# Kernel tuning notes

Measured on AMD Instinct MI355X. Metric: run time of the kernel, lower is better.

## Reference

```python
import jax, jax.numpy as jnp
import numpy as np

B, L, IN_DIM, OUT_DIM = 4, 512, 32, 1
D_MODEL, N_LAYERS = 768, 4
E = 2 * D_MODEL      # d_inner
N = 16               # d_state
K = 4                # d_conv
R = D_MODEL // 16    # dt_rank


def setup_inputs() -> dict:
    key = jax.random.key(0)
    ks = jax.random.split(key, 16)
    p = lambda k, shape, s=0.02: (s * jax.random.normal(k, shape)).astype(jnp.float32)
    inp = {
        'x': jax.random.normal(ks[0], (B, L, IN_DIM), dtype=jnp.float32),
        'in_w': p(ks[1], (D_MODEL, IN_DIM)),
        'in_b': jnp.zeros((D_MODEL,), jnp.float32),
        'in_proj_w': p(ks[2], (N_LAYERS, 2 * E, D_MODEL)),
        'conv_w': p(ks[3], (N_LAYERS, E, K), 0.1),
        'conv_b': jnp.zeros((N_LAYERS, E), jnp.float32),
        'xproj_w': p(ks[4], (N_LAYERS, R + 2 * N, E)),
        'dtproj_w': p(ks[5], (N_LAYERS, E, R), 0.1),
        'dtproj_b': p(ks[6], (N_LAYERS, E), 0.5),
        'A_log': jnp.log(jnp.broadcast_to(jnp.arange(1, N + 1, dtype=jnp.float32), (N_LAYERS, E, N))),
        'D_ssm': jnp.ones((N_LAYERS, E), jnp.float32),
        'outproj_w': p(ks[7], (N_LAYERS, D_MODEL, E)),
        'norm_w': jnp.ones((N_LAYERS, D_MODEL), jnp.float32),
        'normf_w': jnp.ones((D_MODEL,), jnp.float32),
        'out_w': p(ks[8], (OUT_DIM, D_MODEL)),
        'out_b': jnp.zeros((OUT_DIM,), jnp.float32),
    }
    return inp


def _rmsnorm(x, w, eps=1e-5):
    return x * jax.lax.rsqrt(jnp.mean(x * x, axis=-1, keepdims=True) + eps) * w


def _selective_scan(u, delta, A, Bm, C, D):
    # u, delta: [B,L,E]; A: [E,N]; Bm, C: [B,L,N]; D: [E]
    dA = jnp.exp(delta[..., None] * A)                       # [B,L,E,N]
    dBu = delta[..., None] * Bm[:, :, None, :] * u[..., None]  # [B,L,E,N]

    def step(h, inp):
        dA_t, dBu_t, C_t = inp
        h = dA_t * h + dBu_t                                  # [B,E,N]
        y = jnp.einsum('ben,bn->be', h, C_t)
        return h, y

    h0 = jnp.zeros((u.shape[0], u.shape[2], A.shape[1]), u.dtype)
    _, ys = jax.lax.scan(step, h0, (dA.transpose(1, 0, 2, 3), dBu.transpose(1, 0, 2, 3), C.transpose(1, 0, 2)))
    return ys.transpose(1, 0, 2) + u * D                      # [B,L,E]


def _mamba_block(xn, in_proj_w, conv_w, conv_b, xproj_w, dtproj_w, dtproj_b, A_log, D_ssm, outproj_w):
    xz = xn @ in_proj_w.T                                     # [B,L,2E]
    xc, res = xz[..., :E], xz[..., E:]
    # depthwise causal conv1d
    xt = xc.transpose(0, 2, 1)                                # [B,E,L]
    y = jax.lax.conv_general_dilated(xt, conv_w[:, None, :], (1,), [(K - 1, 0)],
                                     feature_group_count=E,
                                     dimension_numbers=('NCH', 'OIH', 'NCH'))
    u = jax.nn.silu((y + conv_b[None, :, None]).transpose(0, 2, 1))  # [B,L,E]
    x_dbl = u @ xproj_w.T                                     # [B,L,R+2N]
    dt, Bm, C = x_dbl[..., :R], x_dbl[..., R:R + N], x_dbl[..., R + N:]
    delta = jax.nn.softplus(dt @ dtproj_w.T + dtproj_b)       # [B,L,E]
    A = -jnp.exp(A_log)                                       # [E,N]
    y = _selective_scan(u, delta, A, Bm, C, D_ssm)
    y = y * jax.nn.silu(res)
    return y @ outproj_w.T                                    # [B,L,D_MODEL]


def reference(x, in_w, in_b, in_proj_w, conv_w, conv_b, xproj_w, dtproj_w, dtproj_b,
              A_log, D_ssm, outproj_w, norm_w, normf_w, out_w, out_b):
    h = x @ in_w.T + in_b                                     # [B,L,D_MODEL]
    for i in range(N_LAYERS):
        h = h + _mamba_block(_rmsnorm(h, norm_w[i]), in_proj_w[i], conv_w[i], conv_b[i],
                             xproj_w[i], dtproj_w[i], dtproj_b[i], A_log[i], D_ssm[i], outproj_w[i])
    h = _rmsnorm(h, normf_w)
    last = h[:, -1, :]
    out = jax.nn.sigmoid(last @ out_w.T + out_b)              # [B,OUT_DIM]
    return out.reshape(-1)
```

## Files before the change

kernel.cpp:

```cpp
#include <hip/hip_runtime.h>
#include <hip/hip_bf16.h>
#include <cmath>

#define BATCH 4
#define SEQ 512
#define TOK (BATCH*SEQ)
#define DMODEL 768
#define EDIM 1536
#define TWOE 3072
#define RDIM 48
#define NSTATE 16
#define RN2 80
#define CONVK 4
#define XSPLIT 6
#define CH 8
#define CL (SEQ/CH)
#define EBLK 64

#define EPI_STORE 0
#define EPI_BIAS 1
#define EPI_BIAS_SOFTPLUS 2
#define EPI_ADD 3

typedef short bf16x8 __attribute__((ext_vector_type(8)));
typedef float f32x4 __attribute__((ext_vector_type(4)));

__device__ __forceinline__ unsigned short f2bf(float f) {
  unsigned int u = __builtin_bit_cast(unsigned int, f);
  u = (u + 0x7FFFu + ((u >> 16) & 1u)) >> 16;
  return (unsigned short)u;
}

template<int BM, int BN, int EPI, bool NB>
__global__ __launch_bounds__(256) void gemm_mfma(
    const unsigned short* __restrict__ Abf,
    const unsigned short* __restrict__ Wbf,
    float* __restrict__ C, int ldc, int Kk, int ldk,
    int Nvalid, size_t zCstride, const float* __restrict__ bias) {
  constexpr int WM = BM / 2, WN = BN / 2;
  constexpr int IT = WM / 16, JT = WN / 16;
  __shared__ __align__(16) char smem[(BM + BN) * 128];
  char* ldsA = smem;
  char* ldsB = smem + BM * 128;

  const int tid = threadIdx.x;
  const int wid = tid >> 6, lane = tid & 63;
  const int m0 = blockIdx.y * BM, n0 = blockIdx.x * BN;
  const int wm = (wid >> 1) * WM, wn = (wid & 1) * WN;
  const int quad = lane >> 4, l15 = lane & 15;

  const int srow = lane >> 3;
  const int kc = (lane & 7) ^ srow;
  const int koff = blockIdx.z * Kk;
  C += (size_t)blockIdx.z * zCstride;
  const unsigned short* gA = Abf + (size_t)(m0 + srow) * ldk + kc * 8 + koff;
  const unsigned short* gB = Wbf + (size_t)(n0 + srow) * ldk + kc * 8 + koff;

  f32x4 acc[IT][JT] = {};

  for (int k0 = 0; k0 < Kk; k0 += 64) {
#pragma unroll
    for (int c = wid; c < BM / 8; c += 4)
      __builtin_amdgcn_global_load_lds(
          (const __attribute__((address_space(1))) void*)(gA + (size_t)(c * 8) * ldk + k0),
          (__attribute__((address_space(3))) void*)(ldsA + c * 1024), 16, 0, 0);
#pragma unroll
    for (int c = wid; c < BN / 8; c += 4)
      __builtin_amdgcn_global_load_lds(
          (const __attribute__((address_space(1))) void*)(gB + (size_t)(c * 8) * ldk + k0),
          (__attribute__((address_space(3))) void*)(ldsB + c * 1024), 16, 0, 0);
    asm volatile("s_waitcnt vmcnt(0)" ::: "memory");
    __syncthreads();
#pragma unroll
    for (int t = 0; t < 2; ++t) {
      const int cc = t * 4 + quad;
      bf16x8 av[IT], bv[JT];
#pragma unroll
      for (int i = 0; i < IT; ++i) {
        const int row = wm + i * 16 + l15;
        const int slot = cc ^ (row & 7);
        av[i] = *(const bf16x8*)(ldsA + row * 128 + slot * 16);
      }
#pragma unroll
      for (int j = 0; j < JT; ++j) {
        const int row = wn + j * 16 + l15;
        const int slot = cc ^ (row & 7);
        bv[j] = *(const bf16x8*)(ldsB + row * 128 + slot * 16);
      }
#pragma unroll
      for (int i = 0; i < IT; ++i)
#pragma unroll
        for (int j = 0; j < JT; ++j)
          acc[i][j] = __builtin_amdgcn_mfma_f32_16x16x32_bf16(av[i], bv[j], acc[i][j], 0, 0, 0);
    }
    __syncthreads();
  }

#pragma unroll
  for (int i = 0; i < IT; ++i) {
#pragma unroll
    for (int r = 0; r < 4; ++r) {
      const int m = m0 + wm + i * 16 + quad * 4 + r;
      float* crow = C + (size_t)m * ldc + n0 + wn;
#pragma unroll
      for (int j = 0; j < JT; ++j) {
        const int n = j * 16 + l15;
        if (NB && (n0 + wn + n) >= Nvalid) continue;
        float v = acc[i][j][r];
        if (EPI == EPI_BIAS_SOFTPLUS) {
          v += bias[n0 + wn + n];
          v = (v > 20.f) ? v : log1pf(expf(v));
        }
        if (EPI == EPI_ADD) v += crow[n];
        crow[n] = v;
      }
    }
  }
}

__global__ __launch_bounds__(256) void reduce_part_k(
    const float* __restrict__ part, float* __restrict__ out,
    unsigned short* __restrict__ dtbf) {
  int i = (blockIdx.x * 256 + threadIdx.x) * 4;
  if (i >= TOK * RN2) return;
  float4 s = *(const float4*)(part + i);
#pragma unroll
  for (int z = 1; z < XSPLIT; ++z) {
    float4 v = *(const float4*)(part + (size_t)z * TOK * RN2 + i);
    s.x += v.x; s.y += v.y; s.z += v.z; s.w += v.w;
  }
  *(float4*)(out + i) = s;
  int row = i / RN2, col = i % RN2;
  if (col < RDIM) {
    ushort4 r;
    r.x = f2bf(s.x); r.y = f2bf(s.y); r.z = f2bf(s.z); r.w = f2bf(s.w);
    *(ushort4*)(dtbf + (size_t)row * 64 + col) = r;
  }
  if (col < 16) {
    ushort4 z0 = {0, 0, 0, 0};
    *(ushort4*)(dtbf + (size_t)row * 64 + RDIM + col) = z0;
  }
}

__global__ __launch_bounds__(256) void cast_dtw_k(
    const float* __restrict__ w, unsigned short* __restrict__ o) {
  int i = (blockIdx.x * 256 + threadIdx.x) * 4;
  if (i >= EDIM * 64) return;
  int row = i / 64, col = i % 64;
  ushort4 r = {0, 0, 0, 0};
  if (col < RDIM) {
    float4 v = *(const float4*)(w + (size_t)row * RDIM + col);
    r.x = f2bf(v.x); r.y = f2bf(v.y); r.z = f2bf(v.z); r.w = f2bf(v.w);
  }
  *(ushort4*)(o + i) = r;
}

template<int EPI>
__global__ __launch_bounds__(256) void gemm_tn(
    const float* __restrict__ A, int lda,
    const float* __restrict__ W, int ldw,
    const float* __restrict__ bias,
    float* __restrict__ C, int ldc,
    int M, int Nn, int Kk) {
  __shared__ float As[16][68];
  __shared__ float Bs[16][68];
  const int tid = threadIdx.x;
  const int m0 = blockIdx.y * 64, n0 = blockIdx.x * 64;
  const int lr = tid >> 2;
  const int lc = (tid & 3) << 2;
  const int ty = tid >> 4, tx = tid & 15;
  float acc[4][4] = {};

  for (int k0 = 0; k0 < Kk; k0 += 16) {
    {
      int m = m0 + lr;
      float4 v = make_float4(0.f, 0.f, 0.f, 0.f);
      if (m < M) v = *(const float4*)(A + (size_t)m * lda + k0 + lc);
      As[lc + 0][lr] = v.x; As[lc + 1][lr] = v.y;
      As[lc + 2][lr] = v.z; As[lc + 3][lr] = v.w;
    }
    {
      int nn = n0 + lr;
      float4 v = make_float4(0.f, 0.f, 0.f, 0.f);
      if (nn < Nn) v = *(const float4*)(W + (size_t)nn * ldw + k0 + lc);
      Bs[lc + 0][lr] = v.x; Bs[lc + 1][lr] = v.y;
      Bs[lc + 2][lr] = v.z; Bs[lc + 3][lr] = v.w;
    }
    __syncthreads();
#pragma unroll
    for (int kk = 0; kk < 16; ++kk) {
      float av[4], bv[4];
#pragma unroll
      for (int i = 0; i < 4; ++i) av[i] = As[kk][ty * 4 + i];
#pragma unroll
      for (int j = 0; j < 4; ++j) bv[j] = Bs[kk][tx * 4 + j];
#pragma unroll
      for (int i = 0; i < 4; ++i)
#pragma unroll
        for (int j = 0; j < 4; ++j)
          acc[i][j] += av[i] * bv[j];
    }
    __syncthreads();
  }

#pragma unroll
  for (int i = 0; i < 4; ++i) {
    int m = m0 + ty * 4 + i;
    if (m >= M) continue;
#pragma unroll
    for (int j = 0; j < 4; ++j) {
      int nn = n0 + tx * 4 + j;
      if (nn >= Nn) continue;
      float v = acc[i][j];
      float* cp = C + (size_t)m * ldc + nn;
      if (EPI == EPI_BIAS) v += bias[nn];
      if (EPI == EPI_ADD) v += *cp;
      *cp = v;
    }
  }
}

__global__ __launch_bounds__(256) void cast_bf16_k(
    const float* __restrict__ w, unsigned short* __restrict__ o, int n) {
  int i = (blockIdx.x * 256 + threadIdx.x) * 4;
  if (i >= n) return;
  float4 v = *(const float4*)(w + i);
  ushort4 r;
  r.x = f2bf(v.x); r.y = f2bf(v.y); r.z = f2bf(v.z); r.w = f2bf(v.w);
  *(ushort4*)(o + i) = r;
}

__global__ __launch_bounds__(256) void rmsnorm_k(
    const float* __restrict__ x, const float* __restrict__ w,
    unsigned short* __restrict__ o, int D) {
  const int t = blockIdx.x;
  const float* row = x + (size_t)t * D;
  __shared__ float ls[8];
  const int lane = threadIdx.x & 63, wave = threadIdx.x >> 6;
  float s = 0.f;
  for (int i = threadIdx.x; i < D; i += 256) { float v = row[i]; s += v * v; }
  for (int off = 32; off; off >>= 1) s += __shfl_down(s, off);
  if (lane == 0) ls[wave] = s;
  __syncthreads();
  float tot = ls[0] + ls[1] + ls[2] + ls[3];
  float rs = rsqrtf(tot / (float)D + 1e-5f);
  for (int i = threadIdx.x; i < D; i += 256)
    o[(size_t)t * D + i] = f2bf(row[i] * rs * w[i]);
}

__global__ __launch_bounds__(256) void conv_silu4_k(
    const float* __restrict__ xz, const float* __restrict__ cw,
    const float* __restrict__ cb, float* __restrict__ u,
    unsigned short* __restrict__ ubf) {
  const int idx = blockIdx.x * 256 + threadIdx.x;
  const int ec = (idx % (EDIM / 4)) * 4;
  const int tok = idx / (EDIM / 4);
  const int tl = tok & (SEQ - 1);
  float4 acc = *(const float4*)(cb + ec);
  float wt[16];
  *(float4*)(wt + 0)  = *(const float4*)(cw + ec * 4);
  *(float4*)(wt + 4)  = *(const float4*)(cw + ec * 4 + 4);
  *(float4*)(wt + 8)  = *(const float4*)(cw + ec * 4 + 8);
  *(float4*)(wt + 12) = *(const float4*)(cw + ec * 4 + 12);
#pragma unroll
  for (int j = 0; j < CONVK; ++j) {
    int tt = tl - (CONVK - 1) + j;
    if (tt >= 0) {
      float4 xv = *(const float4*)(xz + (size_t)(tok - (CONVK - 1) + j) * TWOE + ec);
      acc.x += xv.x * wt[0 * 4 + j];
      acc.y += xv.y * wt[1 * 4 + j];
      acc.z += xv.z * wt[2 * 4 + j];
      acc.w += xv.w * wt[3 * 4 + j];
    }
  }
  float4 s;
  s.x = acc.x / (1.f + __expf(-acc.x));
  s.y = acc.y / (1.f + __expf(-acc.y));
  s.z = acc.z / (1.f + __expf(-acc.z));
  s.w = acc.w / (1.f + __expf(-acc.w));
  *(float4*)(u + (size_t)idx * 4) = s;
  ushort4 r;
  r.x = f2bf(s.x); r.y = f2bf(s.y); r.z = f2bf(s.z); r.w = f2bf(s.w);
  *(ushort4*)(ubf + (size_t)idx * 4) = r;
}


__global__ __launch_bounds__(256) void scan_p1(
    const float* __restrict__ delta, const float* __restrict__ u,
    const float* __restrict__ xdbl, const float* __restrict__ A_log,
    float* __restrict__ hend, float* __restrict__ aprod) {
  const int tid = threadIdx.x;
  const int g = tid >> 2, nq = tid & 3;
  const int nch = blockIdx.x & (CH - 1);
  const int rem = blockIdx.x >> 3;
  const int e0 = (rem % (EDIM / EBLK)) * EBLK;
  const int b = rem / (EDIM / EBLK);
  const int e = e0 + g;
  float4 Al = *(const float4*)(A_log + (size_t)e * NSTATE + nq * 4);
  float4 A4;
  A4.x = -__expf(Al.x); A4.y = -__expf(Al.y);
  A4.z = -__expf(Al.z); A4.w = -__expf(Al.w);
  const size_t base = (size_t)b * SEQ + nch * CL;

  __shared__ float s_dv[2][8][EBLK];
  __shared__ float s_uv[2][8][EBLK];
  __shared__ float s_B[2][8][16];

  const float* gp0 = nullptr; float* ld0 = nullptr; size_t st0 = 0; int off0 = 0;
  const float* gp1 = nullptr; float* ld1 = nullptr; size_t st1 = 0; int off1 = 0;
  if (tid < 128) {
    int j = tid >> 4, q = tid & 15;
    gp0 = delta + (base + j) * EDIM + e0 + q * 4; st0 = 8 * (size_t)EDIM;
    ld0 = &s_dv[0][j][q * 4]; off0 = 8 * EBLK;
    if (tid < 32) {
      int jj = tid >> 2, nn = (tid & 3) * 4;
      gp1 = xdbl + (base + jj) * RN2 + RDIM + nn; st1 = 8 * (size_t)RN2;
      ld1 = &s_B[0][jj][nn]; off1 = 8 * 16;
    }
  } else {
    int r = tid - 128;
    int j = r >> 4, q = r & 15;
    gp0 = u + (base + j) * EDIM + e0 + q * 4; st0 = 8 * (size_t)EDIM;
    ld0 = &s_uv[0][j][q * 4]; off0 = 8 * EBLK;
  }
  if (ld0) { float4 v = *(const float4*)gp0; gp0 += st0; *(float4*)ld0 = v; }
  if (ld1) { float4 v = *(const float4*)gp1; gp1 += st1; *(float4*)ld1 = v; }

  float4 h = {0.f, 0.f, 0.f, 0.f};
  float sdv = 0.f;
  for (int it = 0; it < CL / 8; ++it) {
    const int cur = it & 1;
    const bool hn = (it < CL / 8 - 1);
    float4 nv0, nv1;
    if (hn && ld0) { nv0 = *(const float4*)gp0; gp0 += st0; }
    if (hn && ld1) { nv1 = *(const float4*)gp1; gp1 += st1; }
    __syncthreads();
#pragma unroll
    for (int j = 0; j < 8; ++j) {
      float dv = s_dv[cur][j][g];
      float uv = s_uv[cur][j][g];
      float4 Bv = *(const float4*)&s_B[cur][j][nq * 4];
      float duv = dv * uv;
      h.x = __expf(dv * A4.x) * h.x + duv * Bv.x;
      h.y = __expf(dv * A4.y) * h.y + duv * Bv.y;
      h.z = __expf(dv * A4.z) * h.z + duv * Bv.z;
      h.w = __expf(dv * A4.w) * h.w + duv * Bv.w;
      sdv += dv;
    }
    if (hn && ld0) *(float4*)(ld0 + (cur ^ 1) * off0) = nv0;
    if (hn && ld1) *(float4*)(ld1 + (cur ^ 1) * off1) = nv1;
  }
  size_t o = (((size_t)b * CH + nch) * EDIM + e) * NSTATE + nq * 4;
  *(float4*)(hend + o) = h;
  float4 ap;
  ap.x = __expf(A4.x * sdv); ap.y = __expf(A4.y * sdv);
  ap.z = __expf(A4.z * sdv); ap.w = __expf(A4.w * sdv);
  *(float4*)(aprod + o) = ap;
}

__global__ __launch_bounds__(256) void scan_comb(
    const float* __restrict__ hend, const float* __restrict__ aprod,
    float* __restrict__ hin) {
  int i = blockIdx.x * 256 + threadIdx.x;
  if (i >= BATCH * EDIM * NSTATE) return;
  int b = i / (EDIM * NSTATE);
  int en = i % (EDIM * NSTATE);
  float he[CH], ap[CH];
#pragma unroll
  for (int c = 0; c < CH; ++c) {
    size_t o = ((size_t)(b * CH + c)) * EDIM * NSTATE + en;
    he[c] = hend[o]; ap[c] = aprod[o];
  }
  float hv = 0.f;
#pragma unroll
  for (int c = 0; c < CH; ++c) {
    size_t o = ((size_t)(b * CH + c)) * EDIM * NSTATE + en;
    hin[o] = hv;
    hv = he[c] + ap[c] * hv;
  }
}

__global__ __launch_bounds__(256) void scan_p2(
    const float* __restrict__ delta, const float* __restrict__ u,
    const float* __restrict__ xdbl, const float* __restrict__ xz,
    const float* __restrict__ A_log, const float* __restrict__ D_ssm,
    const float* __restrict__ hin, unsigned short* __restrict__ y) {
  const int tid = threadIdx.x;
  const int g = tid >> 2, nq = tid & 3;
  const int nch = blockIdx.x & (CH - 1);
  const int rem = blockIdx.x >> 3;
  const int e0 = (rem % (EDIM / EBLK)) * EBLK;
  const int b = rem / (EDIM / EBLK);
  const int e = e0 + g;
  float4 Al = *(const float4*)(A_log + (size_t)e * NSTATE + nq * 4);
  float4 A4;
  A4.x = -__expf(Al.x); A4.y = -__expf(Al.y);
  A4.z = -__expf(Al.z); A4.w = -__expf(Al.w);
  const float Dv = D_ssm[e];
  const size_t base = (size_t)b * SEQ + nch * CL;

  __shared__ float s_dv[2][8][EBLK];
  __shared__ float s_uv[2][8][EBLK];
  __shared__ float s_rs[2][8][EBLK];
  __shared__ float s_B[2][8][16];
  __shared__ float s_C[2][8][16];

  const float* gp0 = nullptr; float* ld0 = nullptr; size_t st0 = 0; int off0 = 0;
  const float* gp1 = nullptr; float* ld1 = nullptr; size_t st1 = 0; int off1 = 0;
  if (tid < 128) {
    int j = tid >> 4, q = tid & 15;
    gp0 = delta + (base + j) * EDIM + e0 + q * 4; st0 = 8 * (size_t)EDIM;
    ld0 = &s_dv[0][j][q * 4]; off0 = 8 * EBLK;
    gp1 = xz + (base + j) * TWOE + EDIM + e0 + q * 4; st1 = 8 * (size_t)TWOE;
    ld1 = &s_rs[0][j][q * 4]; off1 = 8 * EBLK;
  } else {
    int r = tid - 128;
    int j = r >> 4, q = r & 15;
    gp0 = u + (base + j) * EDIM + e0 + q * 4; st0 = 8 * (size_t)EDIM;
    ld0 = &s_uv[0][j][q * 4]; off0 = 8 * EBLK;
    if (r < 32) {
      int jj = r >> 2, nn = (r & 3) * 4;
      gp1 = xdbl + (base + jj) * RN2 + RDIM + nn; st1 = 8 * (size_t)RN2;
      ld1 = &s_B[0][jj][nn]; off1 = 8 * 16;
    } else if (r < 64) {
      int r2 = r - 32;
      int jj = r2 >> 2, nn = (r2 & 3) * 4;
      gp1 = xdbl + (base + jj) * RN2 + RDIM + NSTATE + nn; st1 = 8 * (size_t)RN2;
      ld1 = &s_C[0][jj][nn]; off1 = 8 * 16;
    }
  }
  if (ld0) { float4 v = *(const float4*)gp0; gp0 += st0; *(float4*)ld0 = v; }
  if (ld1) { float4 v = *(const float4*)gp1; gp1 += st1; *(float4*)ld1 = v; }

  float4 h = *(const float4*)(hin + (((size_t)b * CH + nch) * EDIM + e) * NSTATE + nq * 4);
  float pva = 0.f, pvb = 0.f;
  unsigned short* yp = y + base * EDIM + e;
  for (int it = 0; it < CL / 8; ++it) {
    const int cur = it & 1;
    const bool hn = (it < CL / 8 - 1);
    float4 nv0, nv1;
    if (hn && ld0) { nv0 = *(const float4*)gp0; gp0 += st0; }
    if (hn && ld1) { nv1 = *(const float4*)gp1; gp1 += st1; }
    __syncthreads();
#pragma unroll
    for (int j = 0; j < 8; ++j) {
      float dv = s_dv[cur][j][g];
      float uv = s_uv[cur][j][g];
      float4 Bv = *(const float4*)&s_B[cur][j][nq * 4];
      float4 Cv = *(const float4*)&s_C[cur][j][nq * 4];
      float duv = dv * uv;
      h.x = __expf(dv * A4.x) * h.x + duv * Bv.x;
      h.y = __expf(dv * A4.y) * h.y + duv * Bv.y;
      h.z = __expf(dv * A4.z) * h.z + duv * Bv.z;
      h.w = __expf(dv * A4.w) * h.w + duv * Bv.w;
      float p = h.x * Cv.x + h.y * Cv.y + h.z * Cv.z + h.w * Cv.w;
      p += __shfl_xor(p, 1);
      p += __shfl_xor(p, 2);
      pva = (j == nq) ? p : pva;
      pvb = (j == nq + 4) ? p : pvb;
    }
    {
      float uv0 = s_uv[cur][nq][g],     rs0 = s_rs[cur][nq][g];
      float uv1 = s_uv[cur][nq + 4][g], rs1 = s_rs[cur][nq + 4][g];
      float sil0 = rs0 / (1.f + __expf(-rs0));
      float sil1 = rs1 / (1.f + __expf(-rs1));
      yp[(size_t)(it * 8 + nq) * EDIM]     = f2bf((pva + uv0 * Dv) * sil0);
      yp[(size_t)(it * 8 + nq + 4) * EDIM] = f2bf((pvb + uv1 * Dv) * sil1);
    }
    if (hn && ld0) *(float4*)(ld0 + (cur ^ 1) * off0) = nv0;
    if (hn && ld1) *(float4*)(ld1 + (cur ^ 1) * off1) = nv1;
  }
}

__global__ __launch_bounds__(256) void final_k(
    const float* __restrict__ h, const float* __restrict__ nw,
    const float* __restrict__ ow, const float* __restrict__ ob,
    float* __restrict__ out) {
  const int b = blockIdx.x;
  const float* row = h + ((size_t)(b * SEQ + SEQ - 1)) * DMODEL;
  __shared__ float ls[8];
  __shared__ float ls2[8];
  const int lane = threadIdx.x & 63, wave = threadIdx.x >> 6;
  float s = 0.f;
  for (int i = threadIdx.x; i < DMODEL; i += 256) { float v = row[i]; s += v * v; }
  for (int off = 32; off; off >>= 1) s += __shfl_down(s, off);
  if (lane == 0) ls[wave] = s;
  __syncthreads();
  float tot = ls[0] + ls[1] + ls[2] + ls[3];
  float rs = rsqrtf(tot / (float)DMODEL + 1e-5f);
  float d = 0.f;
  for (int i = threadIdx.x; i < DMODEL; i += 256)
    d += row[i] * rs * nw[i] * ow[i];
  for (int off = 32; off; off >>= 1) d += __shfl_down(d, off);
  if (lane == 0) ls2[wave] = d;
  __syncthreads();
  if (threadIdx.x == 0) {
    float dot = ls2[0] + ls2[1] + ls2[2] + ls2[3] + ob[0];
    out[b] = 1.f / (1.f + expf(-dot));
  }
}

extern "C" void kernel_launch(void* const* d_in, const int* in_sizes, int n_in,
                              void* d_out, int out_size, void* d_ws, size_t ws_size,
                              hipStream_t stream) {
  const float* x         = (const float*)d_in[0];
  const float* in_w      = (const float*)d_in[1];
  const float* in_b      = (const float*)d_in[2];
  const float* in_proj_w = (const float*)d_in[3];
  const float* conv_w    = (const float*)d_in[4];
  const float* conv_b    = (const float*)d_in[5];
  const float* xproj_w   = (const float*)d_in[6];
  const float* dtproj_w  = (const float*)d_in[7];
  const float* dtproj_b  = (const float*)d_in[8];
  const float* A_log     = (const float*)d_in[9];
  const float* D_ssm     = (const float*)d_in[10];
  const float* outproj_w = (const float*)d_in[11];
  const float* norm_w    = (const float*)d_in[12];
  const float* normf_w   = (const float*)d_in[13];
  const float* out_w     = (const float*)d_in[14];
  const float* out_b     = (const float*)d_in[15];
  float* out = (float*)d_out;
  float* ws  = (float*)d_ws;

  float* h     = ws;
  float* xz    = h + (size_t)TOK * DMODEL;
  float* u     = xz + (size_t)TOK * TWOE;
  float* xdb   = u + (size_t)TOK * EDIM;
  float* dl    = xdb + (size_t)TOK * RN2;
  float* part  = dl + (size_t)TOK * EDIM;
  float* hend  = part + (size_t)XSPLIT * TOK * RN2;
  float* aprod = hend + (size_t)BATCH * CH * EDIM * NSTATE;
  float* hin   = aprod + (size_t)BATCH * CH * EDIM * NSTATE;
  unsigned short* xn_bf = (unsigned short*)(hin + (size_t)BATCH * CH * EDIM * NSTATE);
  unsigned short* y_bf  = xn_bf + (size_t)TOK * DMODEL;
  unsigned short* u_bf  = y_bf + (size_t)TOK * EDIM;
  unsigned short* w_in  = u_bf + (size_t)TOK * EDIM;
  unsigned short* w_out = w_in + (size_t)TWOE * DMODEL;
  unsigned short* w_x   = w_out + (size_t)DMODEL * EDIM;
  unsigned short* dt_bf = w_x + (size_t)128 * EDIM;
  unsigned short* w_dt  = dt_bf + (size_t)TOK * 64;

  dim3 blk(256);

  gemm_tn<EPI_BIAS><<<dim3(DMODEL / 64, TOK / 64), blk, 0, stream>>>(
      x, 32, in_w, 32, in_b, h, DMODEL, TOK, DMODEL, 32);

  for (int l = 0; l < 4; ++l) {
    rmsnorm_k<<<TOK, 256, 0, stream>>>(h, norm_w + l * DMODEL, xn_bf, DMODEL);

    cast_bf16_k<<<(TWOE * DMODEL / 4 + 255) / 256, 256, 0, stream>>>(
        in_proj_w + (size_t)l * TWOE * DMODEL, w_in, TWOE * DMODEL);

    gemm_mfma<128, 128, EPI_STORE, false><<<dim3(TWOE / 128, TOK / 128, 1), blk, 0, stream>>>(
        xn_bf, w_in, xz, TWOE, DMODEL, DMODEL, TWOE, 0, nullptr);

    conv_silu4_k<<<(TOK * EDIM / 4) / 256, 256, 0, stream>>>(
        xz, conv_w + l * EDIM * CONVK, conv_b + l * EDIM, u, u_bf);

    cast_bf16_k<<<(RN2 * EDIM / 4 + 255) / 256, 256, 0, stream>>>(
        xproj_w + (size_t)l * RN2 * EDIM, w_x, RN2 * EDIM);
    gemm_mfma<64, 64, EPI_STORE, true><<<dim3(2, TOK / 64, XSPLIT), blk, 0, stream>>>(
        u_bf, w_x, part, RN2, EDIM / XSPLIT, EDIM, RN2, (size_t)TOK * RN2, nullptr);
    reduce_part_k<<<(TOK * RN2 / 4 + 255) / 256, 256, 0, stream>>>(part, xdb, dt_bf);

    cast_dtw_k<<<(EDIM * 64 / 4 + 255) / 256, 256, 0, stream>>>(
        dtproj_w + (size_t)l * EDIM * RDIM, w_dt);
    gemm_mfma<64, 64, EPI_BIAS_SOFTPLUS, false><<<dim3(EDIM / 64, TOK / 64, 1), blk, 0, stream>>>(
        dt_bf, w_dt, dl, EDIM, 64, 64, EDIM, 0, dtproj_b + l * EDIM);

    scan_p1<<<BATCH * (EDIM / EBLK) * CH, 256, 0, stream>>>(
        dl, u, xdb, A_log + (size_t)l * EDIM * NSTATE, hend, aprod);
    scan_comb<<<(BATCH * EDIM * NSTATE + 255) / 256, 256, 0, stream>>>(
        hend, aprod, hin);
    scan_p2<<<BATCH * (EDIM / EBLK) * CH, 256, 0, stream>>>(
        dl, u, xdb, xz, A_log + (size_t)l * EDIM * NSTATE, D_ssm + l * EDIM,
        hin, y_bf);

    cast_bf16_k<<<(DMODEL * EDIM / 4 + 255) / 256, 256, 0, stream>>>(
        outproj_w + (size_t)l * DMODEL * EDIM, w_out, DMODEL * EDIM);

    gemm_mfma<64, 64, EPI_ADD, false><<<dim3(DMODEL / 64, TOK / 64, 1), blk, 0, stream>>>(
        y_bf, w_out, h, DMODEL, EDIM, EDIM, DMODEL, 0, nullptr);
  }

  final_k<<<BATCH, 256, 0, stream>>>(h, normf_w, out_w, out_b, out);
}
```

Before: 632.5 us.

## Batch weight casts into one kernel, fold scan combine into scan_p2, retile GEMMs

All per-layer fp32-to-bf16 weight casts are merged into a single upfront kernel that converts all four layers into larger workspace buffers, and the x-proj weight padding is now produced by the cast itself. The separate scan_comb kernel is removed; each scan_p2 thread recomputes its chunk's initial state by serially combining the previous chunks' hend/aprod. The dt-proj and out-proj GEMMs switch from 64x64 to 128x64 tiles. Together these cut kernel launches and redundant work, at the cost of more workspace and extra per-thread loads in scan_p2 for later chunks.

```diff
diff --git a/kernel.cpp b/kernel.cpp
--- a/kernel.cpp
+++ b/kernel.cpp
@@ -142,17 +142,46 @@
   }
 }
 
-__global__ __launch_bounds__(256) void cast_dtw_k(
-    const float* __restrict__ w, unsigned short* __restrict__ o) {
-  int i = (blockIdx.x * 256 + threadIdx.x) * 4;
-  if (i >= EDIM * 64) return;
-  int row = i / 64, col = i % 64;
+#define CAST_N1 (4LL*TWOE*DMODEL)
+#define CAST_N2 (4LL*DMODEL*EDIM)
+#define CAST_N3 (4LL*128*EDIM)
+#define CAST_N4 (4LL*EDIM*64)
+#define CAST_TOT (CAST_N1+CAST_N2+CAST_N3+CAST_N4)
+__global__ __launch_bounds__(256) void cast_all_k(
+    const float* __restrict__ inw, const float* __restrict__ outw,
+    const float* __restrict__ xw, const float* __restrict__ dtw,
+    unsigned short* __restrict__ w_in, unsigned short* __restrict__ w_out,
+    unsigned short* __restrict__ w_x, unsigned short* __restrict__ w_dt) {
+  long long i = ((long long)blockIdx.x * 256 + threadIdx.x) * 4;
+  if (i >= CAST_TOT) return;
+  const float* src = nullptr;
+  unsigned short* dst;
+  if (i < CAST_N1) {
+    src = inw + i; dst = w_in + i;
+  } else if (i < CAST_N1 + CAST_N2) {
+    long long j = i - CAST_N1;
+    src = outw + j; dst = w_out + j;
+  } else if (i < CAST_N1 + CAST_N2 + CAST_N3) {
+    long long j = i - CAST_N1 - CAST_N2;
+    int l = (int)(j / (128LL * EDIM));
+    int rem = (int)(j % (128LL * EDIM));
+    int r = rem / EDIM, c = rem % EDIM;
+    dst = w_x + j;
+    if (r < RN2) src = xw + ((long long)l * RN2 + r) * EDIM + c;
+  } else {
+    long long j = i - CAST_N1 - CAST_N2 - CAST_N3;
+    int l = (int)(j / (EDIM * 64LL));
+    int rem = (int)(j % (EDIM * 64LL));
+    int row = rem / 64, col = rem % 64;
+    dst = w_dt + j;
+    if (col < RDIM) src = dtw + ((long long)l * EDIM + row) * RDIM + col;
+  }
   ushort4 r = {0, 0, 0, 0};
-  if (col < RDIM) {
-    float4 v = *(const float4*)(w + (size_t)row * RDIM + col);
+  if (src) {
+    float4 v = *(const float4*)src;
     r.x = f2bf(v.x); r.y = f2bf(v.y); r.z = f2bf(v.z); r.w = f2bf(v.w);
   }
-  *(ushort4*)(o + i) = r;
+  *(ushort4*)dst = r;
 }
 
 template<int EPI>
@@ -218,16 +247,6 @@
       *cp = v;
     }
   }
-}
-
-__global__ __launch_bounds__(256) void cast_bf16_k(
-    const float* __restrict__ w, unsigned short* __restrict__ o, int n) {
-  int i = (blockIdx.x * 256 + threadIdx.x) * 4;
-  if (i >= n) return;
-  float4 v = *(const float4*)(w + i);
-  ushort4 r;
-  r.x = f2bf(v.x); r.y = f2bf(v.y); r.z = f2bf(v.z); r.w = f2bf(v.w);
-  *(ushort4*)(o + i) = r;
 }
 
 __global__ __launch_bounds__(256) void rmsnorm_k(
@@ -358,33 +377,12 @@
   *(float4*)(aprod + o) = ap;
 }
 
-__global__ __launch_bounds__(256) void scan_comb(
-    const float* __restrict__ hend, const float* __restrict__ aprod,
-    float* __restrict__ hin) {
-  int i = blockIdx.x * 256 + threadIdx.x;
-  if (i >= BATCH * EDIM * NSTATE) return;
-  int b = i / (EDIM * NSTATE);
-  int en = i % (EDIM * NSTATE);
-  float he[CH], ap[CH];
-#pragma unroll
-  for (int c = 0; c < CH; ++c) {
-    size_t o = ((size_t)(b * CH + c)) * EDIM * NSTATE + en;
-    he[c] = hend[o]; ap[c] = aprod[o];
-  }
-  float hv = 0.f;
-#pragma unroll
-  for (int c = 0; c < CH; ++c) {
-    size_t o = ((size_t)(b * CH + c)) * EDIM * NSTATE + en;
-    hin[o] = hv;
-    hv = he[c] + ap[c] * hv;
-  }
-}
-
 __global__ __launch_bounds__(256) void scan_p2(
     const float* __restrict__ delta, const float* __restrict__ u,
     const float* __restrict__ xdbl, const float* __restrict__ xz,
     const float* __restrict__ A_log, const float* __restrict__ D_ssm,
-    const float* __restrict__ hin, unsigned short* __restrict__ y) {
+    const float* __restrict__ hend, const float* __restrict__ aprod,
+    unsigned short* __restrict__ y) {
   const int tid = threadIdx.x;
   const int g = tid >> 2, nq = tid & 3;
   const int nch = blockIdx.x & (CH - 1);
@@ -432,7 +430,17 @@
   if (ld0) { float4 v = *(const float4*)gp0; gp0 += st0; *(float4*)ld0 = v; }
   if (ld1) { float4 v = *(const float4*)gp1; gp1 += st1; *(float4*)ld1 = v; }
 
-  float4 h = *(const float4*)(hin + (((size_t)b * CH + nch) * EDIM + e) * NSTATE + nq * 4);
+  float4 h = {0.f, 0.f, 0.f, 0.f};
+  for (int c = 0; c < nch; ++c) {
+    size_t o = (((size_t)b * CH + c) * EDIM + e) * NSTATE + nq * 4;
+    float4 he = *(const float4*)(hend + o);
+    float4 ap = *(const float4*)(aprod + o);
+    h.x = he.x + ap.x * h.x;
+    h.y = he.y + ap.y * h.y;
+    h.z = he.z + ap.z * h.z;
+    h.w = he.w + ap.w * h.w;
+  }
+
   float pva = 0.f, pvb = 0.f;
   unsigned short* yp = y + base * EDIM + e;
   for (int it = 0; it < CL / 8; ++it) {
@@ -530,17 +538,19 @@
   float* part  = dl + (size_t)TOK * EDIM;
   float* hend  = part + (size_t)XSPLIT * TOK * RN2;
   float* aprod = hend + (size_t)BATCH * CH * EDIM * NSTATE;
-  float* hin   = aprod + (size_t)BATCH * CH * EDIM * NSTATE;
-  unsigned short* xn_bf = (unsigned short*)(hin + (size_t)BATCH * CH * EDIM * NSTATE);
+  unsigned short* xn_bf = (unsigned short*)(aprod + (size_t)BATCH * CH * EDIM * NSTATE);
   unsigned short* y_bf  = xn_bf + (size_t)TOK * DMODEL;
   unsigned short* u_bf  = y_bf + (size_t)TOK * EDIM;
-  unsigned short* w_in  = u_bf + (size_t)TOK * EDIM;
-  unsigned short* w_out = w_in + (size_t)TWOE * DMODEL;
-  unsigned short* w_x   = w_out + (size_t)DMODEL * EDIM;
-  unsigned short* dt_bf = w_x + (size_t)128 * EDIM;
-  unsigned short* w_dt  = dt_bf + (size_t)TOK * 64;
+  unsigned short* dt_bf = u_bf + (size_t)TOK * EDIM;
+  unsigned short* w_in  = dt_bf + (size_t)TOK * 64;
+  unsigned short* w_out = w_in + (size_t)4 * TWOE * DMODEL;
+  unsigned short* w_x   = w_out + (size_t)4 * DMODEL * EDIM;
+  unsigned short* w_dt  = w_x + (size_t)4 * 128 * EDIM;
 
   dim3 blk(256);
+
+  cast_all_k<<<(int)((CAST_TOT / 4 + 255) / 256), blk, 0, stream>>>(
+      in_proj_w, outproj_w, xproj_w, dtproj_w, w_in, w_out, w_x, w_dt);
 
   gemm_tn<EPI_BIAS><<<dim3(DMODEL / 64, TOK / 64), blk, 0, stream>>>(
       x, 32, in_w, 32, in_b, h, DMODEL, TOK, DMODEL, 32);
@@ -548,39 +558,29 @@
   for (int l = 0; l < 4; ++l) {
     rmsnorm_k<<<TOK, 256, 0, stream>>>(h, norm_w + l * DMODEL, xn_bf, DMODEL);
 
-    cast_bf16_k<<<(TWOE * DMODEL / 4 + 255) / 256, 256, 0, stream>>>(
-        in_proj_w + (size_t)l * TWOE * DMODEL, w_in, TWOE * DMODEL);
-
     gemm_mfma<128, 128, EPI_STORE, false><<<dim3(TWOE / 128, TOK / 128, 1), blk, 0, stream>>>(
-        xn_bf, w_in, xz, TWOE, DMODEL, DMODEL, TWOE, 0, nullptr);
+        xn_bf, w_in + (size_t)l * TWOE * DMODEL, xz, TWOE, DMODEL, DMODEL, TWOE, 0, nullptr);
 
     conv_silu4_k<<<(TOK * EDIM / 4) / 256, 256, 0, stream>>>(
         xz, conv_w + l * EDIM * CONVK, conv_b + l * EDIM, u, u_bf);
 
-    cast_bf16_k<<<(RN2 * EDIM / 4 + 255) / 256, 256, 0, stream>>>(
-        xproj_w + (size_t)l * RN2 * EDIM, w_x, RN2 * EDIM);
     gemm_mfma<64, 64, EPI_STORE, true><<<dim3(2, TOK / 64, XSPLIT), blk, 0, stream>>>(
-        u_bf, w_x, part, RN2, EDIM / XSPLIT, EDIM, RN2, (size_t)TOK * RN2, nullptr);
+        u_bf, w_x + (size_t)l * 128 * EDIM, part, RN2, EDIM / XSPLIT, EDIM, RN2,
+        (size_t)TOK * RN2, nullptr);
     reduce_part_k<<<(TOK * RN2 / 4 + 255) / 256, 256, 0, stream>>>(part, xdb, dt_bf);
 
-    cast_dtw_k<<<(EDIM * 64 / 4 + 255) / 256, 256, 0, stream>>>(
-        dtproj_w + (size_t)l * EDIM * RDIM, w_dt);
-    gemm_mfma<64, 64, EPI_BIAS_SOFTPLUS, false><<<dim3(EDIM / 64, TOK / 64, 1), blk, 0, stream>>>(
-        dt_bf, w_dt, dl, EDIM, 64, 64, EDIM, 0, dtproj_b + l * EDIM);
+    gemm_mfma<128, 64, EPI_BIAS_SOFTPLUS, false><<<dim3(EDIM / 64, TOK / 128, 1), blk, 0, stream>>>(
+        dt_bf, w_dt + (size_t)l * EDIM * 64, dl, EDIM, 64, 64, EDIM, 0,
+        dtproj_b + l * EDIM);
 
     scan_p1<<<BATCH * (EDIM / EBLK) * CH, 256, 0, stream>>>(
         dl, u, xdb, A_log + (size_t)l * EDIM * NSTATE, hend, aprod);
-    scan_comb<<<(BATCH * EDIM * NSTATE + 255) / 256, 256, 0, stream>>>(
-        hend, aprod, hin);
     scan_p2<<<BATCH * (EDIM / EBLK) * CH, 256, 0, stream>>>(
         dl, u, xdb, xz, A_log + (size_t)l * EDIM * NSTATE, D_ssm + l * EDIM,
-        hin, y_bf);
-
-    cast_bf16_k<<<(DMODEL * EDIM / 4 + 255) / 256, 256, 0, stream>>>(
-        outproj_w + (size_t)l * DMODEL * EDIM, w_out, DMODEL * EDIM);
-
-    gemm_mfma<64, 64, EPI_ADD, false><<<dim3(DMODEL / 64, TOK / 64, 1), blk, 0, stream>>>(
-        y_bf, w_out, h, DMODEL, EDIM, EDIM, DMODEL, 0, nullptr);
+        hend, aprod, y_bf);
+
+    gemm_mfma<128, 64, EPI_ADD, false><<<dim3(DMODEL / 64, TOK / 128, 1), blk, 0, stream>>>(
+        y_bf, w_out + (size_t)l * DMODEL * EDIM, h, DMODEL, EDIM, EDIM, DMODEL, 0, nullptr);
   }
 
   final_k<<<BATCH, 256, 0, stream>>>(h, normf_w, out_w, out_b, out);
```

Measured after the change: 656.8 us. +3.8%, slower.
